# Performance work log

Measured on AMD Instinct MI355X. Metric: run time of the kernel, lower is better.

The kernel has to match this reference:

```python
import jax, jax.numpy as jnp
import numpy as np

N_NODES, N_EDGES, N_GRAPHS, D = 32768, 49152, 1024, 64


def setup_inputs() -> dict:
    key = jax.random.key(0)
    ks = jax.random.split(key, 24)
    p = lambda k, shape, s=0.1: jax.random.normal(k, shape, dtype=jnp.float32) * s
    return dict(
        x=jax.random.normal(ks[0], (N_NODES, 14), dtype=jnp.float32),
        edge_index=jax.random.randint(ks[1], (2, N_EDGES), 0, N_NODES),
        edge_attr=jax.random.uniform(ks[2], (N_EDGES, 4), dtype=jnp.float32),
        batch=jnp.sort(jax.random.randint(ks[3], (N_NODES,), 0, N_GRAPHS)),
        lin0_W=p(ks[4], (D, 14)), lin0_b=p(ks[5], (D,)),
        e1_W=p(ks[6], (128, 4)), e1_b=p(ks[7], (128,)),
        e2_W=p(ks[8], (D * D, 128), 0.02), e2_b=p(ks[9], (D * D,), 0.02),
        root_W=p(ks[10], (D, D)), conv_b=p(ks[11], (D,)),
        gru_Wih=p(ks[12], (3 * D, D)), gru_Whh=p(ks[13], (3 * D, D)),
        gru_bih=p(ks[14], (3 * D,)), gru_bhh=p(ks[15], (3 * D,)),
        lstm_Wih=p(ks[16], (4 * D, 2 * D)), lstm_Whh=p(ks[17], (4 * D, D)),
        lstm_bih=p(ks[18], (4 * D,)), lstm_bhh=p(ks[19], (4 * D,)),
        fc1_W=p(ks[20], (128, 2 * D)), fc1_b=p(ks[21], (128,)),
        fc2_W=p(ks[22], (1, 128)), fc2_b=p(ks[23], (1,)),
    )


def reference(x, edge_index, edge_attr, batch,
              lin0_W, lin0_b, e1_W, e1_b, e2_W, e2_b, root_W, conv_b,
              gru_Wih, gru_Whh, gru_bih, gru_bhh,
              lstm_Wih, lstm_Whh, lstm_bih, lstm_bhh,
              fc1_W, fc1_b, fc2_W, fc2_b):
    N, B = x.shape[0], N_GRAPHS
    src, dst = edge_index[0], edge_index[1]

    out = jax.nn.relu(x @ lin0_W.T + lin0_b)            # [N, D]
    h = out                                             # GRU hidden (num_layers=1)

    # Edge-conditioned weights: edge_attr is constant across the 3 iterations,
    # so compute the edge MLP once (identical math to re-running it).
    W = jax.nn.relu(edge_attr @ e1_W.T + e1_b) @ e2_W.T + e2_b
    W = W.reshape(-1, D, D)                             # [E, D, D]
    cnt = jnp.maximum(
        jax.ops.segment_sum(jnp.ones((src.shape[0],), x.dtype), dst, num_segments=N), 1.0)

    for _ in range(3):
        # NNConv (aggr='mean'): gather -> per-edge matmul -> scatter-mean -> root + bias
        msg = jnp.einsum('ei,eio->eo', out[src], W)     # [E, D]
        agg = jax.ops.segment_sum(msg, dst, num_segments=N) / cnt[:, None]
        m = jax.nn.relu(agg + out @ root_W + conv_b)
        # GRU cell (seq_len=1)
        gi = m @ gru_Wih.T + gru_bih
        gh = h @ gru_Whh.T + gru_bhh
        ir, iz, inn = jnp.split(gi, 3, -1)
        hr, hz, hn = jnp.split(gh, 3, -1)
        r = jax.nn.sigmoid(ir + hr)
        z = jax.nn.sigmoid(iz + hz)
        n = jnp.tanh(inn + r * hn)
        h = (1.0 - z) * n + z * h
        out = h

    # Set2Set pooling, 3 processing steps, LSTM(2D -> D)
    q_star = jnp.zeros((B, 2 * D), x.dtype)
    hl = jnp.zeros((B, D), x.dtype)
    cl = jnp.zeros((B, D), x.dtype)
    for _ in range(3):
        g = q_star @ lstm_Wih.T + lstm_bih + hl @ lstm_Whh.T + lstm_bhh
        i_, f_, g_, o_ = jnp.split(g, 4, -1)
        cl = jax.nn.sigmoid(f_) * cl + jax.nn.sigmoid(i_) * jnp.tanh(g_)
        hl = jax.nn.sigmoid(o_) * jnp.tanh(cl)
        q = hl                                          # [B, D]
        e = jnp.sum(out * q[batch], -1)                 # [N]
        mx = jax.ops.segment_max(e, batch, num_segments=B)
        ex = jnp.exp(e - mx[batch])
        den = jax.ops.segment_sum(ex, batch, num_segments=B)
        a = ex / den[batch]                             # segment softmax
        r_read = jax.ops.segment_sum(a[:, None] * out, batch, num_segments=B)
        q_star = jnp.concatenate([q, r_read], -1)       # [B, 2D]

    hid = jax.nn.relu(q_star @ fc1_W.T + fc1_b)
    return hid @ fc2_W.T + fc2_b                        # [B, 1]
```

## Files before the change

### kernel.cpp

```cpp
#include <hip/hip_runtime.h>
#include <math.h>

#define NN_ 32768
#define NE_ 49152
#define NG_ 1024

typedef short bh8 __attribute__((ext_vector_type(8)));
typedef float f32x4 __attribute__((ext_vector_type(4)));

__device__ __forceinline__ unsigned short f2bfu(float f) {
    union { float f; unsigned int i; } x; x.f = f;
    unsigned int u = x.i;
    u += 0x7FFFu + ((u >> 16) & 1u);
    return (unsigned short)(u >> 16);
}
__device__ __forceinline__ float sigm(float x) { return 1.f / (1.f + expf(-x)); }

__global__ void MPNN_78632261256134_kernel() {}

__global__ void k_zero(float* p, int n) {
    int i = blockIdx.x * 256 + threadIdx.x;
    if (i < n) p[i] = 0.f;
}

__global__ void k_init(float* cnt, float* qstar) {
    int i = blockIdx.x * 256 + threadIdx.x;
    if (i < NN_) cnt[i] = 0.f;
    else if (i < NN_ + NG_ * 256) qstar[i - NN_] = 0.f;
}

__global__ void k_lin0(const float* x, const float* W, const float* b, float* node) {
    int g = blockIdx.x * 256 + threadIdx.x;
    int n = g >> 6, d = g & 63;
    const float* xr = x + n * 14;
    const float* wr = W + d * 14;
    float acc = b[d];
    for (int i = 0; i < 14; i++) acc += xr[i] * wr[i];
    node[g] = fmaxf(acc, 0.f);
}

__global__ void k_cnt(const int* dst, float* cnt) {
    int e = blockIdx.x * 256 + threadIdx.x;
    if (e < NE_) atomicAdd(&cnt[dst[e]], 1.0f);
}

__global__ void k_tw(const float* gWih, const float* gWhh, float* WihT, float* WhhT,
                     const float* lWih, const float* lWhh, float* WihT2, float* WhhT2) {
    int t = blockIdx.x * 256 + threadIdx.x;
    if (t < 12288) {
        int gr = t >> 6, i = t & 63; WihT[i * 192 + gr] = gWih[t];
    } else if (t < 24576) {
        int u = t - 12288; int gr = u >> 6, i = u & 63; WhhT[i * 192 + gr] = gWhh[u];
    } else if (t < 57344) {
        int u = t - 24576; int r = u >> 7, c = u & 127; WihT2[c * 256 + r] = lWih[u];
    } else if (t < 73728) {
        int u = t - 57344; int r = u >> 6, c = u & 63; WhhT2[c * 256 + r] = lWhh[u];
    }
}

__global__ void k_bhat3(const float* e2W, unsigned short* Bhat3) {
    int idx = blockIdx.x * 256 + threadIdx.x;
    if (idx >= 64 * 4 * 4 * 64 * 8) return;
    int j = idx & 7, lane = (idx >> 3) & 63, t = (idx >> 9) & 3, w = (idx >> 11) & 3, s = idx >> 13;
    int row = s * 64 + w * 16 + (lane & 15);
    int k = t * 32 + (lane >> 4) * 8 + j;
    Bhat3[idx] = f2bfu(e2W[row * 128 + k]);
}

__global__ __launch_bounds__(256) void k_he(const float* __restrict__ ea,
                                            const float* __restrict__ e1W,
                                            const float* __restrict__ e1b,
                                            unsigned short* __restrict__ Hhat) {
    int tid = threadIdx.x;
    int lane = tid & 63, sub = tid >> 6;
    int gi = blockIdx.x * 4 + sub;
    int etile = gi >> 2, t = gi & 3;
    int e = etile * 16 + (lane & 15), quad = lane >> 4;
    const float* ar = ea + (size_t)e * 4;
    float a0 = ar[0], a1 = ar[1], a2 = ar[2], a3 = ar[3];
    union { unsigned short u[8]; uint4 q; } o;
#pragma unroll
    for (int j = 0; j < 8; j++) {
        int c = t * 32 + quad * 8 + j;
        const float* wr = e1W + c * 4;
        float h = e1b[c] + a0 * wr[0] + a1 * wr[1] + a2 * wr[2] + a3 * wr[3];
        o.u[j] = f2bfu(fmaxf(h, 0.f));
    }
    *(uint4*)(Hhat + (size_t)gi * 512 + lane * 8) = o.q;
}

__global__ __launch_bounds__(256) void k_convr(const float* __restrict__ node,
                                               const unsigned short* __restrict__ Hhat,
                                               const unsigned short* __restrict__ Bhat3,
                                               const float* __restrict__ e2b,
                                               const int* __restrict__ src,
                                               const int* __restrict__ dst,
                                               float* __restrict__ agg) {
    __shared__ __align__(16) float xs[32 * 68];
    __shared__ int dst_s[64];

    const int tid = threadIdx.x;
    const int bid = blockIdx.x;
    const int etile = bid >> 1, half = bid & 1;
    const int eb = etile * 64;
    const int s0 = half * 32;
    const int lane = tid & 63, w = tid >> 6;
    const int quad = lane >> 4, mrow = lane & 15;

    {
        int r = tid >> 2, c = tid & 3;
        int s = src[eb + r];
        const float* nr = node + (size_t)s * 64 + s0 + c * 8;
#pragma unroll
        for (int j = 0; j < 8; j++) xs[(c * 8 + j) * 68 + r] = nr[j];
        if (tid < 64) dst_s[tid] = dst[eb + tid];
    }

    bh8 af[4][4];
#pragma unroll
    for (int mt = 0; mt < 4; mt++)
#pragma unroll
        for (int t = 0; t < 4; t++)
            af[mt][t] = *(const bh8*)(const void*)(
                Hhat + (size_t)(((eb >> 4) + mt) * 4 + t) * 512 + lane * 8);
    __syncthreads();

    const f32x4 z4 = {0.f, 0.f, 0.f, 0.f};
    f32x4 msg[4];
#pragma unroll
    for (int mt = 0; mt < 4; mt++) msg[mt] = z4;

    bh8 bn[4];
#pragma unroll
    for (int t = 0; t < 4; t++)
        bn[t] = *(const bh8*)(const void*)(Bhat3 + (size_t)((s0 * 4 + w) * 4 + t) * 512 + lane * 8);
    float bbn = e2b[s0 * 64 + w * 16 + mrow];

    for (int s = s0; s < s0 + 32; s++) {
        bh8 bc[4];
#pragma unroll
        for (int t = 0; t < 4; t++) bc[t] = bn[t];
        const float bb = bbn;
        if (s + 1 < s0 + 32) {
#pragma unroll
            for (int t = 0; t < 4; t++)
                bn[t] = *(const bh8*)(const void*)(
                    Bhat3 + (size_t)(((s + 1) * 4 + w) * 4 + t) * 512 + lane * 8);
            bbn = e2b[(s + 1) * 64 + w * 16 + mrow];
        }

        f32x4 acc[4];
#pragma unroll
        for (int t = 0; t < 4; t++)
#pragma unroll
            for (int mt = 0; mt < 4; mt++)
                acc[mt] = __builtin_amdgcn_mfma_f32_16x16x32_bf16(
                    af[mt][t], bc[t], (t == 0) ? z4 : acc[mt], 0, 0, 0);

#pragma unroll
        for (int mt = 0; mt < 4; mt++) {
            f32x4 xv = *(const f32x4*)(const void*)(xs + (s - s0) * 68 + mt * 16 + quad * 4);
#pragma unroll
            for (int r = 0; r < 4; r++)
                msg[mt][r] += xv[r] * (acc[mt][r] + bb);
        }
    }

#pragma unroll
    for (int mt = 0; mt < 4; mt++)
#pragma unroll
        for (int r = 0; r < 4; r++)
            atomicAdd(agg + (size_t)dst_s[mt * 16 + quad * 4 + r] * 64 + w * 16 + mrow,
                      msg[mt][r]);
}

__global__ __launch_bounds__(256) void k_mgru(const float* __restrict__ agg,
                                              const float* __restrict__ cnt,
                                              const float* __restrict__ node,
                                              const float* __restrict__ rootW,
                                              const float* __restrict__ convb,
                                              const float* __restrict__ WihT,
                                              const float* __restrict__ WhhT,
                                              const float* __restrict__ bih,
                                              const float* __restrict__ bhh,
                                              float* __restrict__ hOut) {
    __shared__ __align__(16) float hsT[64][20];
    __shared__ __align__(16) float msT[64][20];
    const int tid = threadIdx.x;
    const int d = tid & 63, sub = tid >> 6;
    const int nb = blockIdx.x * 16;
    const int r0 = sub * 4;

    {
        f32x4 hv;
#pragma unroll
        for (int j = 0; j < 4; j++)
            hv[j] = node[(size_t)(nb + r0 + j) * 64 + d];
        *(f32x4*)&hsT[d][r0] = hv;
    }
    __syncthreads();

    {
        f32x4 root = {0.f, 0.f, 0.f, 0.f};
        for (int i = 0; i < 64; i++) {
            float wv = rootW[i * 64 + d];
            f32x4 h4 = *(const f32x4*)&hsT[i][r0];
#pragma unroll
            for (int j = 0; j < 4; j++) root[j] += h4[j] * wv;
        }
        float cb = convb[d];
        f32x4 mval;
#pragma unroll
        for (int j = 0; j < 4; j++) {
            int n = nb + r0 + j;
            float inv = 1.f / fmaxf(cnt[n], 1.f);
            mval[j] = fmaxf(agg[(size_t)n * 64 + d] * inv + cb + root[j], 0.f);
        }
        *(f32x4*)&msT[d][r0] = mval;
    }
    __syncthreads();

    float ir[4], iz[4], in_[4], hr[4], hz[4], hn[4];
    {
        float bi0 = bih[d], bi1 = bih[64 + d], bi2 = bih[128 + d];
        float bh0 = bhh[d], bh1 = bhh[64 + d], bh2 = bhh[128 + d];
#pragma unroll
        for (int j = 0; j < 4; j++) {
            ir[j] = bi0; iz[j] = bi1; in_[j] = bi2;
            hr[j] = bh0; hz[j] = bh1; hn[j] = bh2;
        }
    }
    for (int i = 0; i < 64; i++) {
        float wi0 = WihT[i * 192 + d];
        float wi1 = WihT[i * 192 + 64 + d];
        float wi2 = WihT[i * 192 + 128 + d];
        float wh0 = WhhT[i * 192 + d];
        float wh1 = WhhT[i * 192 + 64 + d];
        float wh2 = WhhT[i * 192 + 128 + d];
        f32x4 m4 = *(const f32x4*)&msT[i][r0];
        f32x4 h4 = *(const f32x4*)&hsT[i][r0];
#pragma unroll
        for (int j = 0; j < 4; j++) {
            ir[j] += m4[j] * wi0; iz[j] += m4[j] * wi1; in_[j] += m4[j] * wi2;
            hr[j] += h4[j] * wh0; hz[j] += h4[j] * wh1; hn[j] += h4[j] * wh2;
        }
    }
    f32x4 hold = *(const f32x4*)&hsT[d][r0];
#pragma unroll
    for (int j = 0; j < 4; j++) {
        float r = sigm(ir[j] + hr[j]);
        float z = sigm(iz[j] + hz[j]);
        float nn = tanhf(in_[j] + r * hn[j]);
        hOut[(size_t)(nb + r0 + j) * 64 + d] = (1.f - z) * nn + z * hold[j];
    }
}

__global__ __launch_bounds__(64) void k_s2s(const float* __restrict__ node,
                                            const int* __restrict__ batch,
                                            const float* __restrict__ WihT2,
                                            const float* __restrict__ WhhT2,
                                            const float* __restrict__ bih,
                                            const float* __restrict__ bhh,
                                            float* __restrict__ cl,
                                            float* __restrict__ hl,
                                            float* __restrict__ qstar) {
    __shared__ float qvs[128];
    __shared__ float hls[64];
    const int b = blockIdx.x, lane = threadIdx.x;

    qvs[lane] = qstar[(size_t)b * 128 + lane];
    qvs[64 + lane] = qstar[(size_t)b * 128 + 64 + lane];
    hls[lane] = hl[(size_t)b * 64 + lane];
    __syncthreads();

    float acc0 = bih[lane] + bhh[lane];
    float acc1 = bih[64 + lane] + bhh[64 + lane];
    float acc2 = bih[128 + lane] + bhh[128 + lane];
    float acc3 = bih[192 + lane] + bhh[192 + lane];
    for (int j = 0; j < 128; j++) {
        float qj = qvs[j];
        const float* wr = WihT2 + (size_t)j * 256;
        acc0 += qj * wr[lane];
        acc1 += qj * wr[64 + lane];
        acc2 += qj * wr[128 + lane];
        acc3 += qj * wr[192 + lane];
    }
    for (int j = 0; j < 64; j++) {
        float hj = hls[j];
        const float* wr = WhhT2 + (size_t)j * 256;
        acc0 += hj * wr[lane];
        acc1 += hj * wr[64 + lane];
        acc2 += hj * wr[128 + lane];
        acc3 += hj * wr[192 + lane];
    }
    float c = sigm(acc1) * cl[(size_t)b * 64 + lane] + sigm(acc0) * tanhf(acc2);
    cl[(size_t)b * 64 + lane] = c;
    float q = sigm(acc3) * tanhf(c);
    hl[(size_t)b * 64 + lane] = q;

    int lo = 0, hi = NN_;
    while (lo < hi) { int mid = (lo + hi) >> 1; if (batch[mid] < b) lo = mid + 1; else hi = mid; }
    int start = lo;
    lo = start; hi = NN_;
    while (lo < hi) { int mid = (lo + hi) >> 1; if (batch[mid] < b + 1) lo = mid + 1; else hi = mid; }
    int end = lo;

    float r_acc = 0.f, m_run = -1e30f, l_run = 0.f;
    for (int n = start; n < end; n++) {
        float nv = node[(size_t)n * 64 + lane];
        float p = nv * q;
#pragma unroll
        for (int o = 32; o > 0; o >>= 1) p += __shfl_xor(p, o);
        float m_new = fmaxf(m_run, p);
        float sc = expf(m_run - m_new);
        float wgt = expf(p - m_new);
        l_run = l_run * sc + wgt;
        r_acc = r_acc * sc + wgt * nv;
        m_run = m_new;
    }
    qstar[(size_t)b * 128 + lane] = q;
    qstar[(size_t)b * 128 + 64 + lane] = (end > start) ? r_acc / l_run : 0.f;
}

__global__ void k_fc(const float* qstar, const float* W1, const float* b1,
                     const float* W2, const float* b2, float* out) {
    __shared__ float hid[128];
    int b = blockIdx.x; int t = threadIdx.x;
    const float* qr = qstar + (size_t)b * 128;
    float acc = b1[t];
    const float* wr = W1 + (size_t)t * 128;
    for (int k = 0; k < 128; k++) acc += qr[k] * wr[k];
    hid[t] = fmaxf(acc, 0.f);
    __syncthreads();
    if (t < 64) {
        float s = hid[t] * W2[t] + hid[t + 64] * W2[t + 64];
        for (int o = 32; o > 0; o >>= 1) s += __shfl_xor(s, o);
        if (t == 0) out[b] = s + b2[0];
    }
}

extern "C" void kernel_launch(void* const* d_in, const int* in_sizes, int n_in,
                              void* d_out, int out_size, void* d_ws, size_t ws_size,
                              hipStream_t stream) {
    const float* x     = (const float*)d_in[0];
    const int*   ei    = (const int*)d_in[1];
    const float* ea    = (const float*)d_in[2];
    const int*   batch = (const int*)d_in[3];
    const float* lin0W = (const float*)d_in[4];
    const float* lin0b = (const float*)d_in[5];
    const float* e1W   = (const float*)d_in[6];
    const float* e1b   = (const float*)d_in[7];
    const float* e2W   = (const float*)d_in[8];
    const float* e2b   = (const float*)d_in[9];
    const float* rootW = (const float*)d_in[10];
    const float* convb = (const float*)d_in[11];
    const float* gWih  = (const float*)d_in[12];
    const float* gWhh  = (const float*)d_in[13];
    const float* gbih  = (const float*)d_in[14];
    const float* gbhh  = (const float*)d_in[15];
    const float* lWih  = (const float*)d_in[16];
    const float* lWhh  = (const float*)d_in[17];
    const float* lbih  = (const float*)d_in[18];
    const float* lbhh  = (const float*)d_in[19];
    const float* fc1W  = (const float*)d_in[20];
    const float* fc1b  = (const float*)d_in[21];
    const float* fc2W  = (const float*)d_in[22];
    const float* fc2b  = (const float*)d_in[23];
    const int* src = ei;
    const int* dst = ei + NE_;

    char* p = (char*)d_ws;
    auto alloc = [&](size_t bytes) -> char* {
        char* r = p; p += (bytes + 255) & ~(size_t)255; return r;
    };
    unsigned short* Bhat3 = (unsigned short*)alloc((size_t)524288 * 2);
    unsigned short* Hhat  = (unsigned short*)alloc((size_t)NE_ * 128 * 2);
    float* nodeA  = (float*)alloc((size_t)NN_ * 64 * 4);
    float* nodeB  = (float*)alloc((size_t)NN_ * 64 * 4);
    float* aggb   = (float*)alloc((size_t)NN_ * 64 * 4);
    float* cnt    = (float*)alloc((size_t)NN_ * 4);
    float* WihT   = (float*)alloc(192 * 64 * 4);
    float* WhhT   = (float*)alloc(192 * 64 * 4);
    float* WihT2  = (float*)alloc(256 * 128 * 4);
    float* WhhT2  = (float*)alloc(256 * 64 * 4);
    float* qstar  = (float*)alloc((size_t)NG_ * 128 * 4);
    float* hl     = (float*)alloc((size_t)NG_ * 64 * 4);
    float* clb    = (float*)alloc((size_t)NG_ * 64 * 4);

    k_init<<<(NN_ + NG_ * 256 + 255) / 256, 256, 0, stream>>>(cnt, qstar);
    k_lin0<<<NN_ * 64 / 256, 256, 0, stream>>>(x, lin0W, lin0b, nodeA);
    k_cnt<<<NE_ / 256, 256, 0, stream>>>(dst, cnt);
    k_tw<<<288, 256, 0, stream>>>(gWih, gWhh, WihT, WhhT, lWih, lWhh, WihT2, WhhT2);
    k_bhat3<<<524288 / 256, 256, 0, stream>>>(e2W, Bhat3);
    k_he<<<NE_ / 16, 256, 0, stream>>>(ea, e1W, e1b, Hhat);

    float* curF = nodeA; float* nxtF = nodeB;
    for (int it = 0; it < 3; it++) {
        k_zero<<<NN_ * 64 / 256, 256, 0, stream>>>(aggb, NN_ * 64);
        k_convr<<<NE_ / 32, 256, 0, stream>>>(curF, Hhat, Bhat3, e2b, src, dst, aggb);
        k_mgru<<<NN_ / 16, 256, 0, stream>>>(aggb, cnt, curF, rootW, convb,
                                             WihT, WhhT, gbih, gbhh, nxtF);
        float* tf = curF; curF = nxtF; nxtF = tf;
    }

    for (int s = 0; s < 3; s++)
        k_s2s<<<NG_, 64, 0, stream>>>(curF, batch, WihT2, WhhT2, lbih, lbhh, clb, hl, qstar);
    k_fc<<<NG_, 128, 0, stream>>>(qstar, fc1W, fc1b, fc2W, fc2b, (float*)d_out);
}
```

Baseline: 526.9 us.

## Split NNConv work over hidden K-halves instead of input-channel halves

Each block of the fused edge-conv kernel now covers all 64 input channels but only half of the 128-wide hidden dimension, so each step does 2 MFMA K-chunks instead of 4. The bias term is added only by the first half to avoid counting it twice. B-fragment loads are double-buffered two steps at a time, and launch bounds now request 4 blocks per SM. The x tile in shared memory doubles to 64 rows and each block issues twice as many B loads in total, trading that against fewer A registers.

```diff
diff --git a/kernel.cpp b/kernel.cpp
--- a/kernel.cpp
+++ b/kernel.cpp
@@ -89,40 +89,57 @@
     *(uint4*)(Hhat + (size_t)gi * 512 + lane * 8) = o.q;
 }
 
-__global__ __launch_bounds__(256) void k_convr(const float* __restrict__ node,
-                                               const unsigned short* __restrict__ Hhat,
-                                               const unsigned short* __restrict__ Bhat3,
-                                               const float* __restrict__ e2b,
-                                               const int* __restrict__ src,
-                                               const int* __restrict__ dst,
-                                               float* __restrict__ agg) {
-    __shared__ __align__(16) float xs[32 * 68];
+#define CONV_STEP(BREG, BBIAS, SIDX, WITH_BIAS)                                          \
+    {                                                                                    \
+        f32x4 acc[4];                                                                    \
+        _Pragma("unroll")                                                                \
+        for (int mt = 0; mt < 4; mt++)                                                   \
+            acc[mt] = __builtin_amdgcn_mfma_f32_16x16x32_bf16(af[mt][0], BREG[0], z4, 0, 0, 0); \
+        _Pragma("unroll")                                                                \
+        for (int mt = 0; mt < 4; mt++)                                                   \
+            acc[mt] = __builtin_amdgcn_mfma_f32_16x16x32_bf16(af[mt][1], BREG[1], acc[mt], 0, 0, 0); \
+        _Pragma("unroll")                                                                \
+        for (int mt = 0; mt < 4; mt++) {                                                 \
+            f32x4 xv = *(const f32x4*)(const void*)(xs + (SIDX) * 68 + mt * 16 + quad * 4); \
+            _Pragma("unroll")                                                            \
+            for (int r = 0; r < 4; r++)                                                  \
+                msg[mt][r] += xv[r] * (WITH_BIAS ? (acc[mt][r] + (BBIAS)) : acc[mt][r]); \
+        }                                                                                \
+    }
+
+__global__ __launch_bounds__(256, 4) void k_convr(const float* __restrict__ node,
+                                                  const unsigned short* __restrict__ Hhat,
+                                                  const unsigned short* __restrict__ Bhat3,
+                                                  const float* __restrict__ e2b,
+                                                  const int* __restrict__ src,
+                                                  const int* __restrict__ dst,
+                                                  float* __restrict__ agg) {
+    __shared__ __align__(16) float xs[64 * 68];
     __shared__ int dst_s[64];
 
     const int tid = threadIdx.x;
     const int bid = blockIdx.x;
-    const int etile = bid >> 1, half = bid & 1;
+    const int etile = bid >> 1, t0 = bid & 1;
     const int eb = etile * 64;
-    const int s0 = half * 32;
     const int lane = tid & 63, w = tid >> 6;
     const int quad = lane >> 4, mrow = lane & 15;
 
     {
         int r = tid >> 2, c = tid & 3;
         int s = src[eb + r];
-        const float* nr = node + (size_t)s * 64 + s0 + c * 8;
-#pragma unroll
-        for (int j = 0; j < 8; j++) xs[(c * 8 + j) * 68 + r] = nr[j];
+        const float* nr = node + (size_t)s * 64 + c * 16;
+#pragma unroll
+        for (int j = 0; j < 16; j++) xs[(c * 16 + j) * 68 + r] = nr[j];
         if (tid < 64) dst_s[tid] = dst[eb + tid];
     }
 
-    bh8 af[4][4];
+    bh8 af[4][2];
 #pragma unroll
     for (int mt = 0; mt < 4; mt++)
 #pragma unroll
-        for (int t = 0; t < 4; t++)
-            af[mt][t] = *(const bh8*)(const void*)(
-                Hhat + (size_t)(((eb >> 4) + mt) * 4 + t) * 512 + lane * 8);
+        for (int tt = 0; tt < 2; tt++)
+            af[mt][tt] = *(const bh8*)(const void*)(
+                Hhat + (size_t)(((eb >> 4) + mt) * 4 + t0 * 2 + tt) * 512 + lane * 8);
     __syncthreads();
 
     const f32x4 z4 = {0.f, 0.f, 0.f, 0.f};
@@ -130,39 +147,40 @@
 #pragma unroll
     for (int mt = 0; mt < 4; mt++) msg[mt] = z4;
 
-    bh8 bn[4];
-#pragma unroll
-    for (int t = 0; t < 4; t++)
-        bn[t] = *(const bh8*)(const void*)(Bhat3 + (size_t)((s0 * 4 + w) * 4 + t) * 512 + lane * 8);
-    float bbn = e2b[s0 * 64 + w * 16 + mrow];
-
-    for (int s = s0; s < s0 + 32; s++) {
-        bh8 bc[4];
-#pragma unroll
-        for (int t = 0; t < 4; t++) bc[t] = bn[t];
-        const float bb = bbn;
-        if (s + 1 < s0 + 32) {
-#pragma unroll
-            for (int t = 0; t < 4; t++)
-                bn[t] = *(const bh8*)(const void*)(
-                    Bhat3 + (size_t)(((s + 1) * 4 + w) * 4 + t) * 512 + lane * 8);
-            bbn = e2b[(s + 1) * 64 + w * 16 + mrow];
-        }
-
-        f32x4 acc[4];
-#pragma unroll
-        for (int t = 0; t < 4; t++)
-#pragma unroll
-            for (int mt = 0; mt < 4; mt++)
-                acc[mt] = __builtin_amdgcn_mfma_f32_16x16x32_bf16(
-                    af[mt][t], bc[t], (t == 0) ? z4 : acc[mt], 0, 0, 0);
-
-#pragma unroll
-        for (int mt = 0; mt < 4; mt++) {
-            f32x4 xv = *(const f32x4*)(const void*)(xs + (s - s0) * 68 + mt * 16 + quad * 4);
-#pragma unroll
-            for (int r = 0; r < 4; r++)
-                msg[mt][r] += xv[r] * (acc[mt][r] + bb);
+    const unsigned short* __restrict__ bp =
+        Bhat3 + (size_t)(w * 4 + t0 * 2) * 512 + lane * 8;
+
+    bh8 b0[2], b1[2];
+    b0[0] = *(const bh8*)(const void*)(bp);
+    b0[1] = *(const bh8*)(const void*)(bp + 512);
+
+    if (t0 == 0) {
+        const float* __restrict__ ebp = e2b + w * 16 + mrow;
+        float bb0 = ebp[0], bb1;
+        for (int s = 0; s < 64; s += 2) {
+            b1[0] = *(const bh8*)(const void*)(bp + 8192);
+            b1[1] = *(const bh8*)(const void*)(bp + 8192 + 512);
+            bb1 = ebp[64];
+            CONV_STEP(b0, bb0, s, 1)
+            bp += 16384; ebp += 128;
+            if (s + 2 < 64) {
+                b0[0] = *(const bh8*)(const void*)(bp);
+                b0[1] = *(const bh8*)(const void*)(bp + 512);
+                bb0 = ebp[0];
+            }
+            CONV_STEP(b1, bb1, s + 1, 1)
+        }
+    } else {
+        for (int s = 0; s < 64; s += 2) {
+            b1[0] = *(const bh8*)(const void*)(bp + 8192);
+            b1[1] = *(const bh8*)(const void*)(bp + 8192 + 512);
+            CONV_STEP(b0, 0.f, s, 0)
+            bp += 16384;
+            if (s + 2 < 64) {
+                b0[0] = *(const bh8*)(const void*)(bp);
+                b0[1] = *(const bh8*)(const void*)(bp + 512);
+            }
+            CONV_STEP(b1, 0.f, s + 1, 0)
         }
     }
 
```

After: 704.8 us. 1.34x slower.
